# Kernel optimization log

Measured on AMD Instinct MI355X. Metric: run time of the kernel, lower is better.

## Reference

```python
import jax, jax.numpy as jnp
import numpy as np

HID = 2048          # hidden_size
INTER = 4096        # expand * hidden_size
NH = 64             # num_heads
HD = 64             # head_dim (NH*HD == INTER)
N = 128             # ssm state_size
G = 1               # n_groups
K = 4               # conv_kernel
EPS = 1e-5
CONV_DIM = INTER + 2 * G * N            # 4352
PROJ = INTER + CONV_DIM + NH            # 8512 (d_mlp == 0)


def setup_inputs() -> dict:
    key = jax.random.key(0)
    ks = jax.random.split(key, 6)
    B, S = 2, 2048
    return {
        "hidden_states": jax.random.normal(ks[0], (B, S, HID), jnp.float32),
        "in_proj_w": jax.random.normal(ks[1], (PROJ, HID), jnp.float32) * 0.02,
        "conv_w": jax.random.normal(ks[2], (CONV_DIM, 1, K), jnp.float32) * 0.1,
        "conv_b": jax.random.normal(ks[3], (CONV_DIM,), jnp.float32) * 0.02,
        "dt_bias": jnp.ones((NH,), jnp.float32),
        "A_log": jnp.log(jnp.arange(1, NH + 1, dtype=jnp.float32)),
        "D": jnp.ones((NH,), jnp.float32),
        "norm_weight": jnp.ones((INTER,), jnp.float32),
        "out_proj_w": jax.random.normal(ks[4], (HID, INTER), jnp.float32) * 0.02,
    }


def _mamba2_forward(hidden_states, in_proj_w, conv_w, conv_b, dt_bias,
                    A_log, D, norm_weight, out_proj_w):
    b, sq, _ = hidden_states.shape
    # in_proj (d_mlp == 0, so split is gate | hidden_B_C | dt)
    proj = hidden_states @ in_proj_w.T                       # [b, s, PROJ]
    gate, hbc, dt = jnp.split(proj, [INTER, INTER + CONV_DIM], axis=-1)

    # causal depthwise conv1d over time + SiLU
    xc = jnp.transpose(hbc, (0, 2, 1))                       # [b, conv_dim, s]
    xc = jax.lax.conv_general_dilated(xc, conv_w, (1,), [(K - 1, 0)],
                                      feature_group_count=CONV_DIM)
    xc = xc + conv_b[None, :, None]
    hbc = jax.nn.silu(jnp.transpose(xc, (0, 2, 1)))          # [b, s, conv_dim]

    hs, Bm, Cm = jnp.split(hbc, [INTER, INTER + G * N], axis=-1)
    hs = hs.reshape(b, sq, NH, HD)
    Bm = jnp.repeat(Bm.reshape(b, sq, G, N), NH // G, axis=2)   # [b, s, nh, n]
    Cm = jnp.repeat(Cm.reshape(b, sq, G, N), NH // G, axis=2)

    A = -jnp.exp(A_log)                                      # [nh]
    dt = jax.nn.softplus(dt + dt_bias)                       # [b, s, nh]

    # selective SSM scan: state_t = exp(dt*A)*state_{t-1} + dt*B_t x_t^T
    def step(state, inp):
        xt, Bt, Ct, dtt = inp                                # [b,nh,hd],[b,nh,n],[b,nh,n],[b,nh]
        dA = jnp.exp(dtt * A)                                # [b, nh]
        state = state * dA[..., None, None] \
            + (dtt[..., None] * xt)[..., None] * Bt[:, :, None, :]
        y = jnp.einsum('bhdn,bhn->bhd', state, Ct)
        return state, y

    init = jnp.zeros((b, NH, HD, N), jnp.float32)
    xs = (jnp.moveaxis(hs, 1, 0), jnp.moveaxis(Bm, 1, 0),
          jnp.moveaxis(Cm, 1, 0), jnp.moveaxis(dt, 1, 0))
    _, ys = jax.lax.scan(step, init, xs)                     # [s, b, nh, hd]
    y = jnp.moveaxis(ys, 0, 1) + D[None, None, :, None] * hs
    y = y.reshape(b, sq, INTER)

    # gated RMSNorm (norm_before_gate=False): gate first, then normalize
    y = y * jax.nn.silu(gate)
    var = jnp.mean(y * y, axis=-1, keepdims=True)
    y = y * jax.lax.rsqrt(var + EPS) * norm_weight
    return y @ out_proj_w.T                                  # [b, s, HID]


def reference(hidden_states, in_proj_w, conv_w, conv_b, dt_bias, A_log, D,
              norm_weight, out_proj_w):
    return _mamba2_forward(hidden_states, in_proj_w, conv_w, conv_b, dt_bias,
                           A_log, D, norm_weight, out_proj_w)
```

## Files before the change

kernel.cpp:

```cpp
#include <hip/hip_runtime.h>
#include <hip/hip_bf16.h>
#include <cstddef>
#include <cstdint>

#define HID   2048
#define INTER 4096
#define NH    64
#define HD    64
#define NST   128
#define CONV_DIM 4352
#define PROJ  8512
#define PROJ_PAD 8704
#define SS    2048
#define BB    2
#define BS    (BB*SS)
#define EPS   1e-5f

#define COL_HS 4096
#define COL_B  8192
#define COL_C  8320
#define COL_DT 8448

#define NCH   16
#define CHUNK 128

#define CL    128
#define NCHK  16

typedef short s16x8 __attribute__((ext_vector_type(8)));
typedef float f32x4 __attribute__((ext_vector_type(4)));

__device__ inline ushort f2b(float x) {
  __hip_bfloat16 h = __float2bfloat16(x);
  return *(ushort*)&h;
}
__device__ inline float b2f(ushort u) {
  unsigned int v = ((unsigned int)u) << 16;
  return __uint_as_float(v);
}
__device__ inline int swz(int row, int e) { return row * 128 + (e ^ ((row & 7) << 3)); }

__device__ inline void gload16(const void* g, void* l) {
  __builtin_amdgcn_global_load_lds((const __attribute__((address_space(1))) void*)g,
                                   (__attribute__((address_space(3))) void*)l, 16, 0, 0);
}

__global__ __launch_bounds__(256) void to_bf16(const float* __restrict__ src,
                                               ushort* __restrict__ dst, long n4) {
  long i = (long)blockIdx.x * 256 + threadIdx.x;
  if (i >= n4) return;
  float4 v = *(const float4*)(src + i * 4);
  ushort4 o;
  o.x = f2b(v.x); o.y = f2b(v.y); o.z = f2b(v.z); o.w = f2b(v.w);
  *(ushort4*)(dst + i * 4) = o;
}

__global__ __launch_bounds__(256) void to_bf16_pad(const float* __restrict__ src,
                                                   ushort* __restrict__ dst, long n4) {
  long i = (long)blockIdx.x * 256 + threadIdx.x;
  if (i >= n4) return;
  long e0 = i * 4;
  long row = e0 >> 11;
  ushort4 o;
  if (row < PROJ) {
    float4 v = *(const float4*)(src + e0);
    o.x = f2b(v.x); o.y = f2b(v.y); o.z = f2b(v.z); o.w = f2b(v.w);
  } else {
    o.x = o.y = o.z = o.w = 0;
  }
  *(ushort4*)(dst + e0) = o;
}

__global__ __launch_bounds__(512, 2) void gemm256_8ph(
    const ushort* __restrict__ A, const ushort* __restrict__ Bw,
    ushort* __restrict__ C, float* __restrict__ dtbuf) {
  __shared__ ushort smem[65536];
  const int tid = threadIdx.x;
  const int lane = tid & 63;
  const int wid = tid >> 6;
  const int wm = wid >> 2;
  const int wn = wid & 3;
  const int r = lane & 15;
  const int kx = lane >> 4;

  const int fid = blockIdx.x;
  const int bcol = ((fid >> 7) << 3) + ((fid & 127) >> 4);
  const int brow = fid & 15;

  const ushort* Ag = A + (size_t)(brow * 256) * HID;
  const ushort* Bg = Bw + (size_t)(bcol * 256) * HID;

  const int srow = tid >> 3;
  const int scole = (((tid & 7) * 16) ^ ((srow & 7) << 4)) >> 1;

  auto stageA = [&](int buf, int kt, int half) {
    const ushort* g = Ag + (size_t)(half * 128 + srow) * HID + kt * 64 + scole;
    ushort* l = smem + buf * 16384 + half * 8192 + tid * 8;
    gload16(g, l);
    gload16(g + (size_t)64 * HID, l + 4096);
  };
  auto stageB = [&](int buf, int kt, int half) {
    const ushort* g = Bg + (size_t)(half * 128 + srow) * HID + kt * 64 + scole;
    ushort* l = smem + 32768 + buf * 16384 + half * 8192 + tid * 8;
    gload16(g, l);
    gload16(g + (size_t)64 * HID, l + 4096);
  };
  auto ldA = [&](int buf, int mf, int ks) -> s16x8 {
    int row = wm * 128 + mf * 16 + r;
    int cb = (ks * 64 + kx * 16) ^ ((row & 7) << 4);
    return *(const s16x8*)(smem + buf * 16384 + row * 64 + (cb >> 1));
  };
  auto ldB = [&](int buf, int nf, int ks) -> s16x8 {
    int row = wn * 64 + nf * 16 + r;
    int cb = (ks * 64 + kx * 16) ^ ((row & 7) << 4);
    return *(const s16x8*)(smem + 32768 + buf * 16384 + row * 64 + (cb >> 1));
  };

  f32x4 acc[8][4];
#pragma unroll
  for (int i = 0; i < 8; i++)
#pragma unroll
    for (int j = 0; j < 4; j++) acc[i][j] = (f32x4)0.f;

  constexpr int NT = HID / 64;

  stageA(0, 0, 0); stageA(0, 0, 1);
  stageB(0, 0, 0); stageB(0, 0, 1);
  stageA(1, 1, 0); stageA(1, 1, 1);
  asm volatile("s_waitcnt vmcnt(4)" ::: "memory");
  __builtin_amdgcn_s_barrier();

  int cur = 0;
  for (int t = 0; t < NT; t++) {
    s16x8 a[4][2], b[2][2], b2[2][2];
#pragma unroll
    for (int mf = 0; mf < 4; mf++)
#pragma unroll
      for (int ks = 0; ks < 2; ks++) a[mf][ks] = ldA(cur, mf, ks);
#pragma unroll
    for (int nf = 0; nf < 2; nf++)
#pragma unroll
      for (int ks = 0; ks < 2; ks++) b[nf][ks] = ldB(cur, nf, ks);
    if (t + 1 < NT) stageB(cur ^ 1, t + 1, 0);
    __builtin_amdgcn_s_barrier();
    asm volatile("s_waitcnt lgkmcnt(0)" ::: "memory");
    __builtin_amdgcn_sched_barrier(0);
    __builtin_amdgcn_s_setprio(1);
#pragma unroll
    for (int mf = 0; mf < 4; mf++)
#pragma unroll
      for (int nf = 0; nf < 2; nf++)
#pragma unroll
        for (int ks = 0; ks < 2; ks++)
          acc[mf][nf] = __builtin_amdgcn_mfma_f32_16x16x32_bf16(a[mf][ks], b[nf][ks], acc[mf][nf], 0, 0, 0);
    __builtin_amdgcn_s_setprio(0);
    __builtin_amdgcn_s_barrier();
#pragma unroll
    for (int nf = 0; nf < 2; nf++)
#pragma unroll
      for (int ks = 0; ks < 2; ks++) b2[nf][ks] = ldB(cur, nf + 2, ks);
    if (t + 1 < NT) stageB(cur ^ 1, t + 1, 1);
    __builtin_amdgcn_s_barrier();
    asm volatile("s_waitcnt lgkmcnt(0)" ::: "memory");
    __builtin_amdgcn_sched_barrier(0);
    __builtin_amdgcn_s_setprio(1);
#pragma unroll
    for (int mf = 0; mf < 4; mf++)
#pragma unroll
      for (int nf = 0; nf < 2; nf++)
#pragma unroll
        for (int ks = 0; ks < 2; ks++)
          acc[mf][nf + 2] = __builtin_amdgcn_mfma_f32_16x16x32_bf16(a[mf][ks], b2[nf][ks], acc[mf][nf + 2], 0, 0, 0);
    __builtin_amdgcn_s_setprio(0);
    __builtin_amdgcn_s_barrier();
#pragma unroll
    for (int mf = 0; mf < 4; mf++)
#pragma unroll
      for (int ks = 0; ks < 2; ks++) a[mf][ks] = ldA(cur, mf + 4, ks);
    __builtin_amdgcn_s_barrier();
    asm volatile("s_waitcnt lgkmcnt(0)" ::: "memory");
    __builtin_amdgcn_sched_barrier(0);
    __builtin_amdgcn_s_setprio(1);
#pragma unroll
    for (int mf = 0; mf < 4; mf++)
#pragma unroll
      for (int nf = 0; nf < 2; nf++)
#pragma unroll
        for (int ks = 0; ks < 2; ks++)
          acc[mf + 4][nf] = __builtin_amdgcn_mfma_f32_16x16x32_bf16(a[mf][ks], b[nf][ks], acc[mf + 4][nf], 0, 0, 0);
    __builtin_amdgcn_s_setprio(0);
    __builtin_amdgcn_s_barrier();
    if (t + 2 < NT) { stageA(cur, t + 2, 0); stageA(cur, t + 2, 1); }
    __builtin_amdgcn_s_setprio(1);
#pragma unroll
    for (int mf = 0; mf < 4; mf++)
#pragma unroll
      for (int nf = 0; nf < 2; nf++)
#pragma unroll
        for (int ks = 0; ks < 2; ks++)
          acc[mf + 4][nf + 2] = __builtin_amdgcn_mfma_f32_16x16x32_bf16(a[mf][ks], b2[nf][ks], acc[mf + 4][nf + 2], 0, 0, 0);
    __builtin_amdgcn_s_setprio(0);
    if (t + 2 < NT) {
      asm volatile("s_waitcnt vmcnt(4)" ::: "memory");
    } else {
      asm volatile("s_waitcnt vmcnt(0)" ::: "memory");
    }
    __builtin_amdgcn_s_barrier();
    cur ^= 1;
  }

  const int m0 = brow * 256 + wm * 128 + (lane >> 4) * 4;
  const int n0 = bcol * 256 + wn * 64 + r;
#pragma unroll
  for (int mf = 0; mf < 8; mf++) {
#pragma unroll
    for (int nf = 0; nf < 4; nf++) {
      int n = n0 + nf * 16;
      if (n >= PROJ) continue;
#pragma unroll
      for (int q = 0; q < 4; q++) {
        float v = acc[mf][nf][q];
        int m = m0 + mf * 16 + q;
        C[(size_t)m * PROJ + n] = f2b(v);
        if (n >= COL_DT) dtbuf[(size_t)m * 64 + (n - COL_DT)] = v;
      }
    }
  }
}

__global__ __launch_bounds__(512, 2) void gemm2_256x128(
    const ushort* __restrict__ A, const ushort* __restrict__ Bw,
    float* __restrict__ C) {
  __shared__ ushort smem[49152];
  const int tid = threadIdx.x;
  const int lane = tid & 63;
  const int wid = tid >> 6;
  const int wm = wid >> 1;
  const int wn = wid & 1;
  const int r = lane & 15;
  const int kx = lane >> 4;

  const int fid = blockIdx.x;
  const int bcol = fid >> 4;
  const int brow = fid & 15;

  const ushort* Ag = A + (size_t)(brow * 256) * PROJ;
  const ushort* Bg = Bw + (size_t)(bcol * 128) * INTER;

  const int srow = tid >> 3;
  const int scole = (((tid & 7) * 16) ^ ((srow & 7) << 4)) >> 1;

  auto stageA2 = [&](int buf, int kt) {
#pragma unroll
    for (int i = 0; i < 4; i++) {
      gload16(Ag + (size_t)(i * 64 + srow) * PROJ + kt * 64 + scole,
              smem + buf * 16384 + i * 4096 + tid * 8);
    }
  };
  auto stageB2 = [&](int buf, int kt) {
#pragma unroll
    for (int i = 0; i < 2; i++) {
      gload16(Bg + (size_t)(i * 64 + srow) * INTER + kt * 64 + scole,
              smem + 32768 + buf * 8192 + i * 4096 + tid * 8);
    }
  };
  auto ldA2 = [&](int buf, int mf, int ks) -> s16x8 {
    int row = wm * 64 + mf * 16 + r;
    int cb = (ks * 64 + kx * 16) ^ ((row & 7) << 4);
    return *(const s16x8*)(smem + buf * 16384 + row * 64 + (cb >> 1));
  };
  auto ldB2 = [&](int buf, int nf, int ks) -> s16x8 {
    int row = wn * 64 + nf * 16 + r;
    int cb = (ks * 64 + kx * 16) ^ ((row & 7) << 4);
    return *(const s16x8*)(smem + 32768 + buf * 8192 + row * 64 + (cb >> 1));
  };

  f32x4 acc[4][4];
#pragma unroll
  for (int i = 0; i < 4; i++)
#pragma unroll
    for (int j = 0; j < 4; j++) acc[i][j] = (f32x4)0.f;

  constexpr int NT = INTER / 64;

  stageA2(0, 0); stageB2(0, 0);
  stageA2(1, 1); stageB2(1, 1);
  asm volatile("s_waitcnt vmcnt(6)" ::: "memory");
  __builtin_amdgcn_s_barrier();

  int cur = 0;
  for (int t = 0; t < NT; t++) {
    s16x8 a[4][2], b[4][2];
#pragma unroll
    for (int mf = 0; mf < 4; mf++)
#pragma unroll
      for (int ks = 0; ks < 2; ks++) a[mf][ks] = ldA2(cur, mf, ks);
#pragma unroll
    for (int nf = 0; nf < 4; nf++)
#pragma unroll
      for (int ks = 0; ks < 2; ks++) b[nf][ks] = ldB2(cur, nf, ks);
    __builtin_amdgcn_s_barrier();
    asm volatile("s_waitcnt lgkmcnt(0)" ::: "memory");
    __builtin_amdgcn_sched_barrier(0);
    __builtin_amdgcn_s_setprio(1);
#pragma unroll
    for (int mf = 0; mf < 4; mf++)
#pragma unroll
      for (int nf = 0; nf < 2; nf++)
#pragma unroll
        for (int ks = 0; ks < 2; ks++)
          acc[mf][nf] = __builtin_amdgcn_mfma_f32_16x16x32_bf16(a[mf][ks], b[nf][ks], acc[mf][nf], 0, 0, 0);
    __builtin_amdgcn_s_setprio(0);
    __builtin_amdgcn_s_barrier();
    if (t + 2 < NT) { stageA2(cur, t + 2); stageB2(cur, t + 2); }
    __builtin_amdgcn_s_setprio(1);
#pragma unroll
    for (int mf = 0; mf < 4; mf++)
#pragma unroll
      for (int nf = 2; nf < 4; nf++)
#pragma unroll
        for (int ks = 0; ks < 2; ks++)
          acc[mf][nf] = __builtin_amdgcn_mfma_f32_16x16x32_bf16(a[mf][ks], b[nf][ks], acc[mf][nf], 0, 0, 0);
    __builtin_amdgcn_s_setprio(0);
    if (t + 2 < NT) {
      asm volatile("s_waitcnt vmcnt(6)" ::: "memory");
    } else {
      asm volatile("s_waitcnt vmcnt(0)" ::: "memory");
    }
    __builtin_amdgcn_s_barrier();
    cur ^= 1;
  }

  const int m0 = brow * 256 + wm * 64 + (lane >> 4) * 4;
  const int n0 = bcol * 128 + wn * 64 + r;
#pragma unroll
  for (int mf = 0; mf < 4; mf++) {
#pragma unroll
    for (int nf = 0; nf < 4; nf++) {
      int n = n0 + nf * 16;
#pragma unroll
      for (int q = 0; q < 4; q++)
        C[(size_t)(m0 + mf * 16 + q) * HID + n] = acc[mf][nf][q];
    }
  }
}

__global__ void conv_capture(const ushort* __restrict__ proj, ushort* __restrict__ side) {
  int idx = blockIdx.x * 256 + threadIdx.x;
  const int total = BB * CONV_DIM * NCH * 3;
  if (idx >= total) return;
  int c = idx % CONV_DIM;
  int t = idx / CONV_DIM;
  int j = t % 3; t /= 3;
  int chunk = t % NCH;
  int b = t / NCH;
  int s = chunk * CHUNK - 1 - j;
  ushort v = (s >= 0) ? proj[((size_t)b * SS + s) * PROJ + COL_HS + c] : (ushort)0;
  side[((size_t)(b * NCH + chunk) * 3 + j) * CONV_DIM + c] = v;
}

__global__ void conv_silu(ushort* __restrict__ proj, const ushort* __restrict__ side,
                          const float* __restrict__ cw, const float* __restrict__ cb) {
  int idx = blockIdx.x * 256 + threadIdx.x;
  const int total = BB * CONV_DIM * NCH;
  if (idx >= total) return;
  int c = idx % CONV_DIM;
  int t = idx / CONV_DIM;
  int chunk = t % NCH;
  int b = t / NCH;
  float w0 = cw[c * 4 + 0], w1 = cw[c * 4 + 1], w2 = cw[c * 4 + 2], w3 = cw[c * 4 + 3];
  float bias = cb[c];
  const ushort* sd = side + ((size_t)(b * NCH + chunk) * 3) * CONV_DIM;
  float xm1 = b2f(sd[c]);
  float xm2 = b2f(sd[CONV_DIM + c]);
  float xm3 = b2f(sd[2 * CONV_DIM + c]);
  size_t p = ((size_t)b * SS + (size_t)chunk * CHUNK) * PROJ + COL_HS + c;
  for (int s = 0; s < CHUNK; s++) {
    float xin = b2f(proj[p]);
    float o = w3 * xin + w2 * xm1 + w1 * xm2 + w0 * xm3 + bias;
    o = o / (1.f + __expf(-o));
    proj[p] = f2b(o);
    xm3 = xm2; xm2 = xm1; xm1 = xin;
    p += PROJ;
  }
}

__global__ __launch_bounds__(256) void ssd_chunk_state(
    const ushort* __restrict__ proj, const float* __restrict__ dtf,
    const float* __restrict__ dt_bias, const float* __restrict__ A_log,
    ushort* __restrict__ states, float* __restrict__ cumbuf,
    float* __restrict__ dtvbuf) {
  const int bid = blockIdx.x;
  const int c = bid & 15;
  const int h = (bid >> 4) & 63;
  const int b = bid >> 10;
  const int tid = threadIdx.x;
  const int lane = tid & 63;
  const int wv = tid >> 6;
  __shared__ float sdtv[CL], scum[CL], sw[CL];
  __shared__ ushort sBt[128 * 128];
  __shared__ ushort sXw[64 * 128];
  const size_t row0 = (size_t)b * SS + (size_t)c * CL;
  const size_t bh = (size_t)(b * NH + h);

  const float Ah = -__expf(A_log[h]);
  if (tid < CL) {
    float z = dtf[(row0 + tid) * 64 + h] + dt_bias[h];
    float dtv = (z > 20.f) ? z : log1pf(__expf(z));
    sdtv[tid] = dtv;
    sw[tid] = dtv * Ah;
  }
  __syncthreads();
  for (int off = 1; off < CL; off <<= 1) {
    float v = 0.f;
    if (tid < CL) { v = sw[tid]; if (tid >= off) v += sw[tid - off]; }
    __syncthreads();
    if (tid < CL) sw[tid] = v;
    __syncthreads();
  }
  if (tid < CL) {
    scum[tid] = sw[tid];
    cumbuf[bh * SS + c * CL + tid] = sw[tid];
    dtvbuf[bh * SS + c * CL + tid] = sdtv[tid];
  }
  __syncthreads();
  const float cumL = scum[CL - 1];
  if (tid < CL) sw[tid] = __expf(cumL - scum[tid]) * sdtv[tid];
  __syncthreads();

  {
    const int t = tid >> 1, n0 = (tid & 1) * 64;
    const ushort* src = proj + (row0 + t) * PROJ + COL_B + n0;
#pragma unroll
    for (int j = 0; j < 64; j += 8) {
      s16x8 v = *(const s16x8*)(src + j);
#pragma unroll
      for (int e = 0; e < 8; e++) sBt[swz(n0 + j + e, t)] = (ushort)v[e];
    }
  }
  {
    const int d = tid & 63;
    const int t0 = (tid >> 6) * 32;
    for (int t = t0; t < t0 + 32; t++) {
      float x = b2f(proj[(row0 + t) * PROJ + COL_HS + h * 64 + d]);
      sXw[swz(d, t)] = f2b(x * sw[t]);
    }
  }
  __syncthreads();

  const int r = lane & 15, kx = lane >> 4;
  f32x4 acc[2][4];
#pragma unroll
  for (int i = 0; i < 2; i++)
#pragma unroll
    for (int j = 0; j < 4; j++) acc[i][j] = (f32x4)0.f;
#pragma unroll
  for (int kk = 0; kk < 4; kk++) {
    s16x8 a[2], bo[4];
#pragma unroll
    for (int i = 0; i < 2; i++)
      a[i] = *(const s16x8*)&sBt[swz(wv * 32 + i * 16 + r, kk * 32 + kx * 8)];
#pragma unroll
    for (int j = 0; j < 4; j++)
      bo[j] = *(const s16x8*)&sXw[swz(j * 16 + r, kk * 32 + kx * 8)];
#pragma unroll
    for (int i = 0; i < 2; i++)
#pragma unroll
      for (int j = 0; j < 4; j++)
        acc[i][j] = __builtin_amdgcn_mfma_f32_16x16x32_bf16(a[i], bo[j], acc[i][j], 0, 0, 0);
  }
  ushort* dst = states + (size_t)bid * (128 * 64);
#pragma unroll
  for (int i = 0; i < 2; i++) {
#pragma unroll
    for (int j = 0; j < 4; j++) {
      int n = wv * 32 + i * 16 + (lane >> 4) * 4;
      int d = (lane & 15) + j * 16;
      ushort4 o;
      o.x = f2b(acc[i][j][0]);
      o.y = f2b(acc[i][j][1]);
      o.z = f2b(acc[i][j][2]);
      o.w = f2b(acc[i][j][3]);
      *(ushort4*)(dst + (size_t)d * 128 + n) = o;
    }
  }
}

__global__ __launch_bounds__(256) void ssd_state_scan(
    ushort* __restrict__ states, const float* __restrict__ cumbuf) {
  const int bh = blockIdx.x;
  const int tid = threadIdx.x;
  float run[32];
#pragma unroll
  for (int i = 0; i < 32; i++) run[i] = 0.f;
  for (int c = 0; c < NCHK; c++) {
    float dec = __expf(cumbuf[(size_t)bh * SS + c * CL + (CL - 1)]);
    ushort* p = states + ((size_t)bh * NCHK + c) * 8192 + tid * 32;
    s16x8 in[4];
#pragma unroll
    for (int v = 0; v < 4; v++) in[v] = *(const s16x8*)(p + v * 8);
    s16x8 out[4];
#pragma unroll
    for (int v = 0; v < 4; v++) {
#pragma unroll
      for (int e = 0; e < 8; e++) {
        int i = v * 8 + e;
        out[v][e] = (short)f2b(run[i]);
        run[i] = dec * run[i] + b2f((ushort)in[v][e]);
      }
    }
#pragma unroll
    for (int v = 0; v < 4; v++) *(s16x8*)(p + v * 8) = out[v];
  }
}

__global__ __launch_bounds__(256, 2) void ssd_chunk_out(
    ushort* __restrict__ proj, const ushort* __restrict__ states,
    const float* __restrict__ cumbuf, const float* __restrict__ dtvbuf,
    const float* __restrict__ Dp) {
  const int bid = blockIdx.x;
  const int c = bid & 15;
  const int h = (bid >> 4) & 63;
  const int b = bid >> 10;
  const int tid = threadIdx.x;
  const int lane = tid & 63;
  const int wv = tid >> 6;
  __shared__ ushort sC[128 * 128];
  __shared__ ushort sB[128 * 128];
  __shared__ ushort sX[64 * 128];
  const size_t row0 = (size_t)b * SS + (size_t)c * CL;
  const size_t bh = (size_t)(b * NH + h);
  const float* cumb = cumbuf + bh * SS + c * CL;
  const float* dtvb = dtvbuf + bh * SS + c * CL;
  const int r = lane & 15, kx = lane >> 4;

  float ct[2][4];
#pragma unroll
  for (int i = 0; i < 2; i++)
#pragma unroll
    for (int q = 0; q < 4; q++)
      ct[i][q] = cumb[wv * 32 + i * 16 + ((lane >> 4) << 2) + q];
  float cumt[8], dvt[8];
#pragma unroll
  for (int j = 0; j < 8; j++) {
    int tau = j * 16 + (lane & 15);
    cumt[j] = cumb[tau];
    dvt[j] = dtvb[tau];
  }
  const float eC = __expf(cumb[wv * 32 + (lane >> 1)]);

  {
    const int t = tid >> 1, n0 = (tid & 1) * 64;
    const ushort* srcC = proj + (row0 + t) * PROJ + COL_C + n0;
    const ushort* srcB = proj + (row0 + t) * PROJ + COL_B + n0;
#pragma unroll
    for (int j = 0; j < 64; j += 8) {
      *(s16x8*)&sC[swz(t, n0 + j)] = *(const s16x8*)(srcC + j);
      *(s16x8*)&sB[swz(t, n0 + j)] = *(const s16x8*)(srcB + j);
    }
  }
  {
    const int d = tid & 63;
    const int t0 = (tid >> 6) * 32;
    for (int t = t0; t < t0 + 32; t++)
      sX[swz(d, t)] = proj[(row0 + t) * PROJ + COL_HS + h * 64 + d];
  }
  __syncthreads();

  f32x4 g[2][8];
#pragma unroll
  for (int i = 0; i < 2; i++)
#pragma unroll
    for (int j = 0; j < 8; j++) g[i][j] = (f32x4)0.f;
#pragma unroll
  for (int kk = 0; kk < 4; kk++) {
    s16x8 a[2], bo[8];
#pragma unroll
    for (int i = 0; i < 2; i++)
      a[i] = *(const s16x8*)&sC[swz(wv * 32 + i * 16 + r, kk * 32 + kx * 8)];
#pragma unroll
    for (int j = 0; j < 8; j++)
      bo[j] = *(const s16x8*)&sB[swz(j * 16 + r, kk * 32 + kx * 8)];
#pragma unroll
    for (int i = 0; i < 2; i++)
#pragma unroll
      for (int j = 0; j < 8; j++)
        g[i][j] = __builtin_amdgcn_mfma_f32_16x16x32_bf16(a[i], bo[j], g[i][j], 0, 0, 0);
  }

  s16x8 spf[4][4];
  {
    const ushort* sp = states + (size_t)bid * 8192;
#pragma unroll
    for (int kk = 0; kk < 4; kk++)
#pragma unroll
      for (int j = 0; j < 4; j++)
        spf[kk][j] = *(const s16x8*)(sp + (size_t)(j * 16 + r) * 128 + kk * 32 + kx * 8);
  }
  __syncthreads();

#pragma unroll
  for (int j = 0; j < 8; j++) {
    float cu = cumt[j], dv = dvt[j];
    int tau = j * 16 + (lane & 15);
#pragma unroll
    for (int i = 0; i < 2; i++) {
#pragma unroll
      for (int q = 0; q < 4; q++) {
        int t = wv * 32 + i * 16 + ((lane >> 4) << 2) + q;
        float val = (tau <= t) ? g[i][j][q] * __expf(ct[i][q] - cu) * dv : 0.f;
        sB[swz(t, tau)] = f2b(val);
      }
    }
  }
  {
    int t = wv * 32 + (lane >> 1);
    int n0 = (lane & 1) * 64;
#pragma unroll
    for (int j = 0; j < 64; j += 8) {
      s16x8 u = *(const s16x8*)&sC[swz(t, n0 + j)];
#pragma unroll
      for (int k = 0; k < 8; k++) u[k] = (short)f2b(b2f((ushort)u[k]) * eC);
      *(s16x8*)&sC[swz(t, n0 + j)] = u;
    }
  }
  __syncthreads();

  f32x4 y[2][4];
#pragma unroll
  for (int i = 0; i < 2; i++)
#pragma unroll
    for (int j = 0; j < 4; j++) y[i][j] = (f32x4)0.f;
#pragma unroll
  for (int kk = 0; kk < 4; kk++) {
    s16x8 a[2], bo[4];
#pragma unroll
    for (int i = 0; i < 2; i++)
      a[i] = *(const s16x8*)&sB[swz(wv * 32 + i * 16 + r, kk * 32 + kx * 8)];
#pragma unroll
    for (int j = 0; j < 4; j++)
      bo[j] = *(const s16x8*)&sX[swz(j * 16 + r, kk * 32 + kx * 8)];
#pragma unroll
    for (int i = 0; i < 2; i++)
#pragma unroll
      for (int j = 0; j < 4; j++)
        y[i][j] = __builtin_amdgcn_mfma_f32_16x16x32_bf16(a[i], bo[j], y[i][j], 0, 0, 0);
  }
#pragma unroll
  for (int kk = 0; kk < 4; kk++) {
    s16x8 a[2];
#pragma unroll
    for (int i = 0; i < 2; i++)
      a[i] = *(const s16x8*)&sC[swz(wv * 32 + i * 16 + r, kk * 32 + kx * 8)];
#pragma unroll
    for (int i = 0; i < 2; i++)
#pragma unroll
      for (int j = 0; j < 4; j++)
        y[i][j] = __builtin_amdgcn_mfma_f32_16x16x32_bf16(a[i], spf[kk][j], y[i][j], 0, 0, 0);
  }

  const float Dh = Dp[h];
#pragma unroll
  for (int i = 0; i < 2; i++) {
#pragma unroll
    for (int j = 0; j < 4; j++) {
      int t0 = wv * 32 + i * 16 + (lane >> 4) * 4;
      int d = (lane & 15) + j * 16;
#pragma unroll
      for (int q = 0; q < 4; q++) {
        float x = b2f(sX[swz(d, t0 + q)]);
        proj[(row0 + t0 + q) * PROJ + COL_HS + h * 64 + d] = f2b(y[i][j][q] + Dh * x);
      }
    }
  }
}

__global__ __launch_bounds__(256) void rmsnorm_kernel(
    ushort* __restrict__ proj, const float* __restrict__ nw) {
  const int row = blockIdx.x;
  const int tid = threadIdx.x;
  ushort* yp = proj + (size_t)row * PROJ + COL_HS;
  const ushort* gp = proj + (size_t)row * PROJ;
  float v[16];
  float ss = 0.f;
#pragma unroll
  for (int q = 0; q < 4; q++) {
    int col = q * 1024 + tid * 4;
    ushort4 yv = *(const ushort4*)(yp + col);
    ushort4 gv = *(const ushort4*)(gp + col);
    float vy[4] = {b2f(yv.x), b2f(yv.y), b2f(yv.z), b2f(yv.w)};
    float vg[4] = {b2f(gv.x), b2f(gv.y), b2f(gv.z), b2f(gv.w)};
#pragma unroll
    for (int j = 0; j < 4; j++) {
      float sg = vg[j] / (1.f + __expf(-vg[j]));
      float vv = vy[j] * sg;
      v[q * 4 + j] = vv;
      ss += vv * vv;
    }
  }
#pragma unroll
  for (int o = 1; o < 64; o <<= 1) ss += __shfl_xor(ss, o);
  __shared__ float red[4];
  if ((tid & 63) == 0) red[tid >> 6] = ss;
  __syncthreads();
  float tot = red[0] + red[1] + red[2] + red[3];
  float scale = rsqrtf(tot * (1.f / INTER) + EPS);
#pragma unroll
  for (int q = 0; q < 4; q++) {
    int col = q * 1024 + tid * 4;
    float4 w = *(const float4*)(nw + col);
    ushort4 o;
    o.x = f2b(v[q * 4 + 0] * scale * w.x);
    o.y = f2b(v[q * 4 + 1] * scale * w.y);
    o.z = f2b(v[q * 4 + 2] * scale * w.z);
    o.w = f2b(v[q * 4 + 3] * scale * w.w);
    *(ushort4*)(yp + col) = o;
  }
}

extern "C" void kernel_launch(void* const* d_in, const int* in_sizes, int n_in,
                              void* d_out, int out_size, void* d_ws, size_t ws_size,
                              hipStream_t stream) {
  const float* hs   = (const float*)d_in[0];
  const float* w1   = (const float*)d_in[1];
  const float* cw   = (const float*)d_in[2];
  const float* cb   = (const float*)d_in[3];
  const float* dtb  = (const float*)d_in[4];
  const float* alog = (const float*)d_in[5];
  const float* Dp   = (const float*)d_in[6];
  const float* nw   = (const float*)d_in[7];
  const float* w2   = (const float*)d_in[8];
  float* out = (float*)d_out;

  char* base = (char*)d_ws;
  size_t off = 0;
  ushort* proj = (ushort*)(base + off); off += (size_t)BS * PROJ * 2;
  ushort* side = (ushort*)(base + off); off += (size_t)BB * NCH * 3 * CONV_DIM * 2;
  off = (off + 255) & ~(size_t)255;
  float* dtbuf = (float*)(base + off); off += (size_t)BS * 64 * 4;
  off = (off + 255) & ~(size_t)255;
  char* rC = base + off;
  ushort* hs16 = (ushort*)rC;
  ushort* w1p  = (ushort*)(rC + 16777216);
  ushort* states = (ushort*)rC;
  float*  cumbuf = (float*)(rC + 33554432);
  float*  dtvbuf = (float*)(rC + 33554432 + 1048576);
  ushort* w216 = (ushort*)rC;

  {
    long n4 = (long)BS * HID / 4;
    to_bf16<<<(n4 + 255) / 256, 256, 0, stream>>>(hs, hs16, n4);
  }
  {
    long n4 = (long)PROJ_PAD * HID / 4;
    to_bf16_pad<<<(n4 + 255) / 256, 256, 0, stream>>>(w1, w1p, n4);
  }

  gemm256_8ph<<<(BS / 256) * (PROJ_PAD / 256), 512, 0, stream>>>(hs16, w1p, proj, dtbuf);

  conv_capture<<<(BB * CONV_DIM * NCH * 3 + 255) / 256, 256, 0, stream>>>(proj, side);
  conv_silu<<<(BB * CONV_DIM * NCH + 255) / 256, 256, 0, stream>>>(proj, side, cw, cb);

  ssd_chunk_state<<<BB * NH * NCHK, 256, 0, stream>>>(proj, dtbuf, dtb, alog, states, cumbuf, dtvbuf);
  ssd_state_scan<<<BB * NH, 256, 0, stream>>>(states, cumbuf);
  ssd_chunk_out<<<BB * NH * NCHK, 256, 0, stream>>>(proj, states, cumbuf, dtvbuf, Dp);

  {
    long n4 = (long)HID * INTER / 4;
    to_bf16<<<(n4 + 255) / 256, 256, 0, stream>>>(w2, w216, n4);
  }

  rmsnorm_kernel<<<BS, 256, 0, stream>>>(proj, nw);

  gemm2_256x128<<<256, 512, 0, stream>>>(
      (const ushort*)(proj + COL_HS), w216, out);
}
```

Baseline: 441.4 us.

## Fuse bf16 conversions, retile in_proj GEMM to 256x128, vectorize conv

New measurement: 440.1 us. Within noise of the previous version (-0.3%).

```diff
diff --git a/kernel.cpp b/kernel.cpp
--- a/kernel.cpp
+++ b/kernel.cpp
@@ -21,8 +21,9 @@
 #define COL_C  8320
 #define COL_DT 8448
 
-#define NCH   16
-#define CHUNK 128
+#define NCHC  64
+#define CHUNKC 32
+#define CV8   (CONV_DIM / 8)
 
 #define CL    128
 #define NCHK  16
@@ -45,103 +46,115 @@
                                    (__attribute__((address_space(3))) void*)l, 16, 0, 0);
 }
 
-__global__ __launch_bounds__(256) void to_bf16(const float* __restrict__ src,
-                                               ushort* __restrict__ dst, long n4) {
+#define N4A  ((long)BS * HID / 4)
+#define N4W1 ((long)PROJ_PAD * HID / 4)
+#define N4W2 ((long)HID * INTER / 4)
+
+__global__ __launch_bounds__(256) void convert_all(
+    const float* __restrict__ hs, const float* __restrict__ w1,
+    const float* __restrict__ w2, ushort* __restrict__ hs16,
+    ushort* __restrict__ w1p, ushort* __restrict__ w216) {
   long i = (long)blockIdx.x * 256 + threadIdx.x;
-  if (i >= n4) return;
-  float4 v = *(const float4*)(src + i * 4);
+  const float* src;
+  ushort* dst;
+  long e0;
+  if (i < N4A) {
+    src = hs; dst = hs16; e0 = i * 4;
+  } else if (i < N4A + N4W1) {
+    long k = i - N4A;
+    e0 = k * 4;
+    long row = e0 >> 11;
+    if (row >= PROJ) {
+      ushort4 z = {0, 0, 0, 0};
+      *(ushort4*)(w1p + e0) = z;
+      return;
+    }
+    src = w1; dst = w1p;
+  } else if (i < N4A + N4W1 + N4W2) {
+    long k = i - N4A - N4W1;
+    src = w2; dst = w216; e0 = k * 4;
+  } else {
+    return;
+  }
+  float4 v = *(const float4*)(src + e0);
   ushort4 o;
   o.x = f2b(v.x); o.y = f2b(v.y); o.z = f2b(v.z); o.w = f2b(v.w);
-  *(ushort4*)(dst + i * 4) = o;
-}
-
-__global__ __launch_bounds__(256) void to_bf16_pad(const float* __restrict__ src,
-                                                   ushort* __restrict__ dst, long n4) {
-  long i = (long)blockIdx.x * 256 + threadIdx.x;
-  if (i >= n4) return;
-  long e0 = i * 4;
-  long row = e0 >> 11;
-  ushort4 o;
-  if (row < PROJ) {
-    float4 v = *(const float4*)(src + e0);
-    o.x = f2b(v.x); o.y = f2b(v.y); o.z = f2b(v.z); o.w = f2b(v.w);
-  } else {
-    o.x = o.y = o.z = o.w = 0;
-  }
   *(ushort4*)(dst + e0) = o;
 }
 
-__global__ __launch_bounds__(512, 2) void gemm256_8ph(
+__global__ __launch_bounds__(512, 2) void gemm1_256x128(
     const ushort* __restrict__ A, const ushort* __restrict__ Bw,
     ushort* __restrict__ C, float* __restrict__ dtbuf) {
-  __shared__ ushort smem[65536];
+  __shared__ ushort smem[49152];
   const int tid = threadIdx.x;
   const int lane = tid & 63;
   const int wid = tid >> 6;
-  const int wm = wid >> 2;
-  const int wn = wid & 3;
+  const int wm = wid >> 1;
+  const int wn = wid & 1;
   const int r = lane & 15;
   const int kx = lane >> 4;
 
   const int fid = blockIdx.x;
-  const int bcol = ((fid >> 7) << 3) + ((fid & 127) >> 4);
-  const int brow = fid & 15;
+  const int rg = fid / 272;
+  const int ix = fid % 272;
+  const int brow = rg * 4 + (ix & 3);
+  const int bcol = ix >> 2;
 
   const ushort* Ag = A + (size_t)(brow * 256) * HID;
-  const ushort* Bg = Bw + (size_t)(bcol * 256) * HID;
+  const ushort* Bg = Bw + (size_t)(bcol * 128) * HID;
 
   const int srow = tid >> 3;
   const int scole = (((tid & 7) * 16) ^ ((srow & 7) << 4)) >> 1;
 
-  auto stageA = [&](int buf, int kt, int half) {
-    const ushort* g = Ag + (size_t)(half * 128 + srow) * HID + kt * 64 + scole;
-    ushort* l = smem + buf * 16384 + half * 8192 + tid * 8;
-    gload16(g, l);
-    gload16(g + (size_t)64 * HID, l + 4096);
+  auto stageA1 = [&](int buf, int kt) {
+#pragma unroll
+    for (int i = 0; i < 4; i++) {
+      gload16(Ag + (size_t)(i * 64 + srow) * HID + kt * 64 + scole,
+              smem + buf * 16384 + i * 4096 + tid * 8);
+    }
   };
-  auto stageB = [&](int buf, int kt, int half) {
-    const ushort* g = Bg + (size_t)(half * 128 + srow) * HID + kt * 64 + scole;
-    ushort* l = smem + 32768 + buf * 16384 + half * 8192 + tid * 8;
-    gload16(g, l);
-    gload16(g + (size_t)64 * HID, l + 4096);
+  auto stageB1 = [&](int buf, int kt) {
+#pragma unroll
+    for (int i = 0; i < 2; i++) {
+      gload16(Bg + (size_t)(i * 64 + srow) * HID + kt * 64 + scole,
+              smem + 32768 + buf * 8192 + i * 4096 + tid * 8);
+    }
   };
-  auto ldA = [&](int buf, int mf, int ks) -> s16x8 {
-    int row = wm * 128 + mf * 16 + r;
+  auto ldA1 = [&](int buf, int mf, int ks) -> s16x8 {
+    int row = wm * 64 + mf * 16 + r;
     int cb = (ks * 64 + kx * 16) ^ ((row & 7) << 4);
     return *(const s16x8*)(smem + buf * 16384 + row * 64 + (cb >> 1));
   };
-  auto ldB = [&](int buf, int nf, int ks) -> s16x8 {
+  auto ldB1 = [&](int buf, int nf, int ks) -> s16x8 {
     int row = wn * 64 + nf * 16 + r;
     int cb = (ks * 64 + kx * 16) ^ ((row & 7) << 4);
-    return *(const s16x8*)(smem + 32768 + buf * 16384 + row * 64 + (cb >> 1));
+    return *(const s16x8*)(smem + 32768 + buf * 8192 + row * 64 + (cb >> 1));
   };
 
-  f32x4 acc[8][4];
-#pragma unroll
-  for (int i = 0; i < 8; i++)
+  f32x4 acc[4][4];
+#pragma unroll
+  for (int i = 0; i < 4; i++)
 #pragma unroll
     for (int j = 0; j < 4; j++) acc[i][j] = (f32x4)0.f;
 
   constexpr int NT = HID / 64;
 
-  stageA(0, 0, 0); stageA(0, 0, 1);
-  stageB(0, 0, 0); stageB(0, 0, 1);
-  stageA(1, 1, 0); stageA(1, 1, 1);
-  asm volatile("s_waitcnt vmcnt(4)" ::: "memory");
+  stageA1(0, 0); stageB1(0, 0);
+  stageA1(1, 1); stageB1(1, 1);
+  asm volatile("s_waitcnt vmcnt(6)" ::: "memory");
   __builtin_amdgcn_s_barrier();
 
   int cur = 0;
   for (int t = 0; t < NT; t++) {
-    s16x8 a[4][2], b[2][2], b2[2][2];
+    s16x8 a[4][2], b[4][2];
 #pragma unroll
     for (int mf = 0; mf < 4; mf++)
 #pragma unroll
-      for (int ks = 0; ks < 2; ks++) a[mf][ks] = ldA(cur, mf, ks);
-#pragma unroll
-    for (int nf = 0; nf < 2; nf++)
-#pragma unroll
-      for (int ks = 0; ks < 2; ks++) b[nf][ks] = ldB(cur, nf, ks);
-    if (t + 1 < NT) stageB(cur ^ 1, t + 1, 0);
+      for (int ks = 0; ks < 2; ks++) a[mf][ks] = ldA1(cur, mf, ks);
+#pragma unroll
+    for (int nf = 0; nf < 4; nf++)
+#pragma unroll
+      for (int ks = 0; ks < 2; ks++) b[nf][ks] = ldB1(cur, nf, ks);
     __builtin_amdgcn_s_barrier();
     asm volatile("s_waitcnt lgkmcnt(0)" ::: "memory");
     __builtin_amdgcn_sched_barrier(0);
@@ -155,53 +168,18 @@
           acc[mf][nf] = __builtin_amdgcn_mfma_f32_16x16x32_bf16(a[mf][ks], b[nf][ks], acc[mf][nf], 0, 0, 0);
     __builtin_amdgcn_s_setprio(0);
     __builtin_amdgcn_s_barrier();
-#pragma unroll
-    for (int nf = 0; nf < 2; nf++)
-#pragma unroll
-      for (int ks = 0; ks < 2; ks++) b2[nf][ks] = ldB(cur, nf + 2, ks);
-    if (t + 1 < NT) stageB(cur ^ 1, t + 1, 1);
-    __builtin_amdgcn_s_barrier();
-    asm volatile("s_waitcnt lgkmcnt(0)" ::: "memory");
-    __builtin_amdgcn_sched_barrier(0);
+    if (t + 2 < NT) { stageA1(cur, t + 2); stageB1(cur, t + 2); }
     __builtin_amdgcn_s_setprio(1);
 #pragma unroll
     for (int mf = 0; mf < 4; mf++)
 #pragma unroll
-      for (int nf = 0; nf < 2; nf++)
+      for (int nf = 2; nf < 4; nf++)
 #pragma unroll
         for (int ks = 0; ks < 2; ks++)
-          acc[mf][nf + 2] = __builtin_amdgcn_mfma_f32_16x16x32_bf16(a[mf][ks], b2[nf][ks], acc[mf][nf + 2], 0, 0, 0);
-    __builtin_amdgcn_s_setprio(0);
-    __builtin_amdgcn_s_barrier();
-#pragma unroll
-    for (int mf = 0; mf < 4; mf++)
-#pragma unroll
-      for (int ks = 0; ks < 2; ks++) a[mf][ks] = ldA(cur, mf + 4, ks);
-    __builtin_amdgcn_s_barrier();
-    asm volatile("s_waitcnt lgkmcnt(0)" ::: "memory");
-    __builtin_amdgcn_sched_barrier(0);
-    __builtin_amdgcn_s_setprio(1);
-#pragma unroll
-    for (int mf = 0; mf < 4; mf++)
-#pragma unroll
-      for (int nf = 0; nf < 2; nf++)
-#pragma unroll
-        for (int ks = 0; ks < 2; ks++)
-          acc[mf + 4][nf] = __builtin_amdgcn_mfma_f32_16x16x32_bf16(a[mf][ks], b[nf][ks], acc[mf + 4][nf], 0, 0, 0);
-    __builtin_amdgcn_s_setprio(0);
-    __builtin_amdgcn_s_barrier();
-    if (t + 2 < NT) { stageA(cur, t + 2, 0); stageA(cur, t + 2, 1); }
-    __builtin_amdgcn_s_setprio(1);
-#pragma unroll
-    for (int mf = 0; mf < 4; mf++)
-#pragma unroll
-      for (int nf = 0; nf < 2; nf++)
-#pragma unroll
-        for (int ks = 0; ks < 2; ks++)
-          acc[mf + 4][nf + 2] = __builtin_amdgcn_mfma_f32_16x16x32_bf16(a[mf][ks], b2[nf][ks], acc[mf + 4][nf + 2], 0, 0, 0);
+          acc[mf][nf] = __builtin_amdgcn_mfma_f32_16x16x32_bf16(a[mf][ks], b[nf][ks], acc[mf][nf], 0, 0, 0);
     __builtin_amdgcn_s_setprio(0);
     if (t + 2 < NT) {
-      asm volatile("s_waitcnt vmcnt(4)" ::: "memory");
+      asm volatile("s_waitcnt vmcnt(6)" ::: "memory");
     } else {
       asm volatile("s_waitcnt vmcnt(0)" ::: "memory");
     }
@@ -209,10 +187,10 @@
     cur ^= 1;
   }
 
-  const int m0 = brow * 256 + wm * 128 + (lane >> 4) * 4;
-  const int n0 = bcol * 256 + wn * 64 + r;
-#pragma unroll
-  for (int mf = 0; mf < 8; mf++) {
+  const int m0 = brow * 256 + wm * 64 + (lane >> 4) * 4;
+  const int n0 = bcol * 128 + wn * 64 + r;
+#pragma unroll
+  for (int mf = 0; mf < 4; mf++) {
 #pragma unroll
     for (int nf = 0; nf < 4; nf++) {
       int n = n0 + nf * 16;
@@ -345,42 +323,65 @@
   }
 }
 
-__global__ void conv_capture(const ushort* __restrict__ proj, ushort* __restrict__ side) {
+__global__ __launch_bounds__(256) void conv_capture(
+    const ushort* __restrict__ proj, ushort* __restrict__ side) {
   int idx = blockIdx.x * 256 + threadIdx.x;
-  const int total = BB * CONV_DIM * NCH * 3;
+  const int total = BB * NCHC * 3 * CV8;
   if (idx >= total) return;
-  int c = idx % CONV_DIM;
-  int t = idx / CONV_DIM;
+  int c8 = idx % CV8;
+  int t = idx / CV8;
   int j = t % 3; t /= 3;
-  int chunk = t % NCH;
-  int b = t / NCH;
-  int s = chunk * CHUNK - 1 - j;
-  ushort v = (s >= 0) ? proj[((size_t)b * SS + s) * PROJ + COL_HS + c] : (ushort)0;
-  side[((size_t)(b * NCH + chunk) * 3 + j) * CONV_DIM + c] = v;
-}
-
-__global__ void conv_silu(ushort* __restrict__ proj, const ushort* __restrict__ side,
-                          const float* __restrict__ cw, const float* __restrict__ cb) {
+  int chunk = t % NCHC;
+  int b = t / NCHC;
+  int s = chunk * CHUNKC - 1 - j;
+  s16x8 v = {0, 0, 0, 0, 0, 0, 0, 0};
+  if (s >= 0) v = *(const s16x8*)(proj + ((size_t)b * SS + s) * PROJ + COL_HS + c8 * 8);
+  *(s16x8*)(side + ((size_t)(b * NCHC + chunk) * 3 + j) * CONV_DIM + c8 * 8) = v;
+}
+
+__global__ __launch_bounds__(256) void conv_silu(
+    ushort* __restrict__ proj, const ushort* __restrict__ side,
+    const float* __restrict__ cw, const float* __restrict__ cb) {
   int idx = blockIdx.x * 256 + threadIdx.x;
-  const int total = BB * CONV_DIM * NCH;
+  const int total = BB * NCHC * CV8;
   if (idx >= total) return;
-  int c = idx % CONV_DIM;
-  int t = idx / CONV_DIM;
-  int chunk = t % NCH;
-  int b = t / NCH;
-  float w0 = cw[c * 4 + 0], w1 = cw[c * 4 + 1], w2 = cw[c * 4 + 2], w3 = cw[c * 4 + 3];
-  float bias = cb[c];
-  const ushort* sd = side + ((size_t)(b * NCH + chunk) * 3) * CONV_DIM;
-  float xm1 = b2f(sd[c]);
-  float xm2 = b2f(sd[CONV_DIM + c]);
-  float xm3 = b2f(sd[2 * CONV_DIM + c]);
-  size_t p = ((size_t)b * SS + (size_t)chunk * CHUNK) * PROJ + COL_HS + c;
-  for (int s = 0; s < CHUNK; s++) {
-    float xin = b2f(proj[p]);
-    float o = w3 * xin + w2 * xm1 + w1 * xm2 + w0 * xm3 + bias;
-    o = o / (1.f + __expf(-o));
-    proj[p] = f2b(o);
-    xm3 = xm2; xm2 = xm1; xm1 = xin;
+  int c8 = idx % CV8;
+  int t = idx / CV8;
+  int chunk = t % NCHC;
+  int b = t / NCHC;
+  const int c0 = c8 * 8;
+  float w0[8], w1[8], w2[8], w3[8], bias[8], h1[8], h2[8], h3[8];
+#pragma unroll
+  for (int e = 0; e < 8; e++) {
+    float4 wv = *(const float4*)(cw + (c0 + e) * 4);
+    w0[e] = wv.x; w1[e] = wv.y; w2[e] = wv.z; w3[e] = wv.w;
+    bias[e] = cb[c0 + e];
+  }
+  const ushort* sd = side + (size_t)(b * NCHC + chunk) * 3 * CONV_DIM;
+  {
+    s16x8 v1 = *(const s16x8*)(sd + c0);
+    s16x8 v2 = *(const s16x8*)(sd + CONV_DIM + c0);
+    s16x8 v3 = *(const s16x8*)(sd + 2 * CONV_DIM + c0);
+#pragma unroll
+    for (int e = 0; e < 8; e++) {
+      h1[e] = b2f((ushort)v1[e]);
+      h2[e] = b2f((ushort)v2[e]);
+      h3[e] = b2f((ushort)v3[e]);
+    }
+  }
+  size_t p = ((size_t)b * SS + (size_t)chunk * CHUNKC) * PROJ + COL_HS + c0;
+  for (int s = 0; s < CHUNKC; s++) {
+    s16x8 xv = *(const s16x8*)(proj + p);
+    s16x8 ov;
+#pragma unroll
+    for (int e = 0; e < 8; e++) {
+      float x = b2f((ushort)xv[e]);
+      float o = w3[e] * x + w2[e] * h1[e] + w1[e] * h2[e] + w0[e] * h3[e] + bias[e];
+      o = o / (1.f + __expf(-o));
+      ov[e] = (short)f2b(o);
+      h3[e] = h2[e]; h2[e] = h1[e]; h1[e] = x;
+    }
+    *(s16x8*)(proj + p) = ov;
     p += PROJ;
   }
 }
@@ -735,9 +736,11 @@
   char* base = (char*)d_ws;
   size_t off = 0;
   ushort* proj = (ushort*)(base + off); off += (size_t)BS * PROJ * 2;
-  ushort* side = (ushort*)(base + off); off += (size_t)BB * NCH * 3 * CONV_DIM * 2;
+  ushort* side = (ushort*)(base + off); off += (size_t)BB * NCHC * 3 * CONV_DIM * 2;
   off = (off + 255) & ~(size_t)255;
   float* dtbuf = (float*)(base + off); off += (size_t)BS * 64 * 4;
+  off = (off + 255) & ~(size_t)255;
+  ushort* w216 = (ushort*)(base + off); off += (size_t)HID * INTER * 2;
   off = (off + 255) & ~(size_t)255;
   char* rC = base + off;
   ushort* hs16 = (ushort*)rC;
@@ -745,31 +748,21 @@
   ushort* states = (ushort*)rC;
   float*  cumbuf = (float*)(rC + 33554432);
   float*  dtvbuf = (float*)(rC + 33554432 + 1048576);
-  ushort* w216 = (ushort*)rC;
 
   {
-    long n4 = (long)BS * HID / 4;
-    to_bf16<<<(n4 + 255) / 256, 256, 0, stream>>>(hs, hs16, n4);
-  }
-  {
-    long n4 = (long)PROJ_PAD * HID / 4;
-    to_bf16_pad<<<(n4 + 255) / 256, 256, 0, stream>>>(w1, w1p, n4);
-  }
-
-  gemm256_8ph<<<(BS / 256) * (PROJ_PAD / 256), 512, 0, stream>>>(hs16, w1p, proj, dtbuf);
-
-  conv_capture<<<(BB * CONV_DIM * NCH * 3 + 255) / 256, 256, 0, stream>>>(proj, side);
-  conv_silu<<<(BB * CONV_DIM * NCH + 255) / 256, 256, 0, stream>>>(proj, side, cw, cb);
+    long n4 = N4A + N4W1 + N4W2;
+    convert_all<<<(int)((n4 + 255) / 256), 256, 0, stream>>>(hs, w1, w2, hs16, w1p, w216);
+  }
+
+  gemm1_256x128<<<1088, 512, 0, stream>>>(hs16, w1p, proj, dtbuf);
+
+  conv_capture<<<(BB * NCHC * 3 * CV8 + 255) / 256, 256, 0, stream>>>(proj, side);
+  conv_silu<<<(BB * NCHC * CV8 + 255) / 256, 256, 0, stream>>>(proj, side, cw, cb);
 
   ssd_chunk_state<<<BB * NH * NCHK, 256, 0, stream>>>(proj, dtbuf, dtb, alog, states, cumbuf, dtvbuf);
   ssd_state_scan<<<BB * NH, 256, 0, stream>>>(states, cumbuf);
   ssd_chunk_out<<<BB * NH * NCHK, 256, 0, stream>>>(proj, states, cumbuf, dtvbuf, Dp);
 
-  {
-    long n4 = (long)HID * INTER / 4;
-    to_bf16<<<(n4 + 255) / 256, 256, 0, stream>>>(w2, w216, n4);
-  }
-
   rmsnorm_kernel<<<BS, 256, 0, stream>>>(proj, nw);
 
   gemm2_256x128<<<256, 512, 0, stream>>>(
```
